# Kernel tuning notes

Hardware: AMD Instinct MI355X
Metric: run time of the kernel (lower is better)

Reference implementation:

```python
import jax, jax.numpy as jnp
import numpy as np

# dims: N batch, C in-channels, T frames, V joints, H heads, HD per-head dim, O out-channels
N, C, T, V = 32, 64, 256, 25
H, HD, O = 8, 8, 64  # HD = max(C//8, 8)
SCALE = HD ** -0.5
EPS = 1e-5


def setup_inputs() -> dict:
    key = jax.random.key(0)
    ks = jax.random.split(key, 10)
    return {
        "x": jax.random.normal(ks[0], (N, C, T, V), jnp.float32),
        "ln_gamma": jnp.ones((C,), jnp.float32),
        "ln_beta": jnp.zeros((C,), jnp.float32),
        "w_qk": jax.random.normal(ks[1], (C, 2 * H * HD), jnp.float32),  # to_qk init N(0,1)
        "b_qk": jax.random.normal(ks[2], (2 * H * HD,), jnp.float32) * 0.02,
        "shared_topology": jax.random.uniform(ks[3], (H, V, V), jnp.float32),
        "conv_w": jax.random.normal(ks[4], (H, O, C), jnp.float32) * np.sqrt(2.0 / (O * H)),
        "conv_b": jnp.zeros((H, O), jnp.float32),
        "bn_gamma": jnp.full((O,), 1e-6, jnp.float32),
        "bn_beta": jnp.zeros((O,), jnp.float32),
        "bn_mean": jnp.zeros((O,), jnp.float32),
        "bn_var": jnp.ones((O,), jnp.float32),
    }


def reference(x, ln_gamma, ln_beta, w_qk, b_qk, shared_topology,
              conv_w, conv_b, bn_gamma, bn_beta, bn_mean, bn_var):
    # ---- SelfAttention over joints ----
    y = jnp.transpose(x, (0, 2, 3, 1))                 # [N,T,V,C]
    mu = jnp.mean(y, axis=-1, keepdims=True)
    var = jnp.var(y, axis=-1, keepdims=True)
    yn = (y - mu) * jax.lax.rsqrt(var + EPS) * ln_gamma + ln_beta
    qk = yn @ w_qk + b_qk                              # [N,T,V,2*H*HD]
    B = N * T
    q, k = jnp.split(qk.reshape(B, V, 2 * H * HD), 2, axis=-1)
    q = q.reshape(B, V, H, HD).transpose(0, 2, 1, 3)   # [B,H,V,HD]
    k = k.reshape(B, V, H, HD).transpose(0, 2, 1, 3)
    dots = jnp.einsum("bhid,bhjd->bhij", q, k) * SCALE
    attn = jax.nn.softmax(dots, axis=-1).astype(jnp.float32)  # [B,H,V,V]

    # ---- attention-gated graph conv ----
    A = attn * shared_topology[None]                   # [B,H,V,V]
    feat = jnp.transpose(x, (0, 2, 3, 1)).reshape(B, V, C)  # [B,V,C]
    z = jnp.einsum("bhuv,bvc->bhuc", A, feat)          # per-head aggregate [B,H,V,C]
    # fused per-head 1x1 convs + sum over heads
    out = jnp.einsum("bhuc,hoc->buo", z, conv_w) + conv_b.sum(0)  # [B,V,O]
    out = out.reshape(N, T, V, O).transpose(0, 3, 1, 2)           # [N,O,T,V]

    # ---- BatchNorm (inference-mode) + residual + ReLU ----
    g = (bn_gamma * jax.lax.rsqrt(bn_var + EPS))[None, :, None, None]
    b = (bn_beta - bn_mean * bn_gamma * jax.lax.rsqrt(bn_var + EPS))[None, :, None, None]
    out = out * g + b
    out = jax.nn.relu(out + x)  # down is identity (in_c == out_c)
    return out
```

## Files before the change

kernel.cpp:

```cpp
#include <hip/hip_runtime.h>
#include <math.h>

#define SCALE 0.35355339059327373f
#define EPSV 1e-5f

typedef __attribute__((ext_vector_type(8))) short bf16x8;
typedef __attribute__((ext_vector_type(4))) float f32x4;
typedef __attribute__((ext_vector_type(16))) float f32x16;
typedef __attribute__((ext_vector_type(4))) int i32x4;
typedef __attribute__((ext_vector_type(2))) int i32x2;

static __device__ __forceinline__ unsigned short bfh(float f) {
    return (unsigned short)(__builtin_bit_cast(unsigned int, f) >> 16);
}
static __device__ __forceinline__ float bf2f(unsigned short s) {
    return __builtin_bit_cast(float, (unsigned int)s << 16);
}
static __device__ __forceinline__ int pack2(float lo, float hi) {
    return __builtin_amdgcn_perm(__builtin_bit_cast(unsigned int, hi),
                                 __builtin_bit_cast(unsigned int, lo), 0x07060302u);
}
#define LGKM0() __asm__ __volatile__("s_waitcnt lgkmcnt(0)" ::: "memory")

__global__ void prep_kernel(const float* __restrict__ w_qk,
                            const float* __restrict__ conv_w,
                            const float* __restrict__ conv_b,
                            const float* __restrict__ bn_g, const float* __restrict__ bn_b,
                            const float* __restrict__ bn_m, const float* __restrict__ bn_v,
                            unsigned short* __restrict__ ws) {
    int i = blockIdx.x * 256 + threadIdx.x;
    if (i < 8192) {
        int f = i >> 9, rem = i & 511, l = rem >> 3, j = rem & 7;
        int nt = f >> 1, ks = f & 1;
        int k = ks * 32 + (l >> 4) * 8 + j;
        int nn = nt * 16 + (l & 15);
        ws[i] = bfh(w_qk[k * 128 + nn]);
    } else if (i < 40960) {
        int i2 = i - 8192;
        int g = i2 >> 9, rem = i2 & 511, l = rem >> 3, j = rem & 7;
        int h = g >> 3, nt = (g >> 1) & 3, ks = g & 1;
        int c = ks * 32 + (l >> 4) * 8 + j;
        int o = nt * 16 + (l & 15);
        ws[i] = bfh(conv_w[h * 4096 + o * 64 + c]);
    } else if (i < 41024) {
        int o = i - 40960;
        float gv = bn_g[o] * rsqrtf(bn_v[o] + EPSV);
        float bb = bn_b[o] - bn_m[o] * gv;
        float cb = 0.f;
        for (int h = 0; h < 8; h++) cb += conv_b[h * 64 + o];
        float* wsf = (float*)(ws + 40960);
        wsf[o] = gv;
        wsf[64 + o] = bb + cb * gv;
    }
}

__global__ __launch_bounds__(256, 3)
void sagc_kernel(const float* __restrict__ x,
                 const float* __restrict__ ln_g, const float* __restrict__ ln_b,
                 const float* __restrict__ b_qk,
                 const float* __restrict__ topo,
                 const unsigned short* __restrict__ ws,
                 float* __restrict__ out)
{
    __shared__ __align__(16) unsigned char smem[53248];
    const int tid = threadIdx.x;
    const int lane = tid & 63, wv = tid >> 6;
    const int l15 = lane & 15, quad = lane >> 4;
    const int r32 = lane & 31, hi = lane >> 5;

    unsigned char* my = smem + wv * 13312;
    unsigned short* xb16 = (unsigned short*)my;
    unsigned short* FWT  = (unsigned short*)my;
    float*          mus  = (float*)(my + 5120);
    float*          rss  = mus + 32;
    unsigned short* qbuf = (unsigned short*)(my + 5120);
    unsigned short* kbuf = (unsigned short*)(my + 6656);
    unsigned short* Gh   = (unsigned short*)(my + 8192);

    const unsigned short* wqk = ws;
    const unsigned short* w2f = ws + 8192;
    const float* bnA = (const float*)(ws + 40960);
    const float* bnB = bnA + 64;

    const int tile = blockIdx.x * 4 + wv;
    const int n = tile >> 8, t = tile & 255;
    const float* xg = x + (size_t)n * 409600 + (size_t)t * 25;
    float* og = out + (size_t)n * 409600 + (size_t)t * 25;

    #pragma unroll
    for (int it = 0; it < 25; it++) {
        int i = it * 64 + lane;
        int c = i / 25, v = i - c * 25;
        xb16[v * 72 + c] = bfh(xg[c * 6400 + v]);
    }
    #pragma unroll
    for (int k = 0; k < 8; k++) {
        int idx = k * 64 + lane;
        if (idx < 504) {
            int rr = idx / 72, cc = idx - rr * 72;
            xb16[(25 + rr) * 72 + cc] = 0;
        }
    }
    LGKM0();

    bf16x8 xa[2][2];
    #pragma unroll
    for (int mt = 0; mt < 2; mt++)
        #pragma unroll
        for (int ks = 0; ks < 2; ks++)
            xa[mt][ks] = *(const bf16x8*)&xb16[(mt * 16 + l15) * 72 + ks * 32 + quad * 8];

    float xf[2][2][8];
    bf16x8 sqf[2][2];
    #pragma unroll
    for (int mt = 0; mt < 2; mt++)
        #pragma unroll
        for (int ks = 0; ks < 2; ks++) {
            float s[8];
            #pragma unroll
            for (int j = 0; j < 8; j++) {
                xf[mt][ks][j] = bf2f((unsigned short)xa[mt][ks][j]);
                s[j] = xf[mt][ks][j] * xf[mt][ks][j];
            }
            i32x4 p;
            #pragma unroll
            for (int q = 0; q < 4; q++) p[q] = pack2(s[2 * q], s[2 * q + 1]);
            sqf[mt][ks] = __builtin_bit_cast(bf16x8, p);
        }

    {
        i32x4 ones_i = {0x3C803C80, 0x3C803C80, 0x3C803C80, 0x3C803C80};
        bf16x8 onesf = __builtin_bit_cast(bf16x8, ones_i);
        f32x4 z4 = {0.f, 0.f, 0.f, 0.f};
        f32x4 dmu[2], ds2[2];
        #pragma unroll
        for (int mt = 0; mt < 2; mt++) {
            dmu[mt] = __builtin_amdgcn_mfma_f32_16x16x32_bf16(xa[mt][0], onesf, z4, 0, 0, 0);
            dmu[mt] = __builtin_amdgcn_mfma_f32_16x16x32_bf16(xa[mt][1], onesf, dmu[mt], 0, 0, 0);
            ds2[mt] = __builtin_amdgcn_mfma_f32_16x16x32_bf16(sqf[mt][0], onesf, z4, 0, 0, 0);
            ds2[mt] = __builtin_amdgcn_mfma_f32_16x16x32_bf16(sqf[mt][1], onesf, ds2[mt], 0, 0, 0);
        }
        if (l15 == 0) {
            #pragma unroll
            for (int mt = 0; mt < 2; mt++)
                #pragma unroll
                for (int r = 0; r < 4; r++) {
                    int v = mt * 16 + quad * 4 + r;
                    float mu = dmu[mt][r];
                    float var = ds2[mt][r] - mu * mu;
                    mus[v] = mu;
                    rss[v] = rsqrtf(var + EPSV);
                }
        }
    }
    LGKM0();

    bf16x8 yna[2][2];
    {
        float muv[2] = {mus[l15], mus[16 + l15]};
        float rsv[2] = {rss[l15], rss[16 + l15]};
        #pragma unroll
        for (int ks = 0; ks < 2; ks++) {
            f32x4 ga = *(const f32x4*)&ln_g[ks * 32 + quad * 8];
            f32x4 gb = *(const f32x4*)&ln_g[ks * 32 + quad * 8 + 4];
            f32x4 ba = *(const f32x4*)&ln_b[ks * 32 + quad * 8];
            f32x4 bb = *(const f32x4*)&ln_b[ks * 32 + quad * 8 + 4];
            #pragma unroll
            for (int mt = 0; mt < 2; mt++) {
                float yv[8];
                #pragma unroll
                for (int j = 0; j < 8; j++) {
                    float g = (j < 4) ? ga[j] : gb[j - 4];
                    float bt = (j < 4) ? ba[j] : bb[j - 4];
                    yv[j] = (xf[mt][ks][j] - muv[mt]) * rsv[mt] * g + bt;
                }
                i32x4 p;
                #pragma unroll
                for (int q = 0; q < 4; q++) p[q] = pack2(yv[2 * q], yv[2 * q + 1]);
                yna[mt][ks] = __builtin_bit_cast(bf16x8, p);
            }
        }
    }

    f32x4 acc[2][4];
    #pragma unroll
    for (int mt = 0; mt < 2; mt++)
        #pragma unroll
        for (int nt = 0; nt < 4; nt++)
            acc[mt][nt] = (f32x4){0.f, 0.f, 0.f, 0.f};

    const f32x4 z4 = {0.f, 0.f, 0.f, 0.f};
    const bf16x8 z8 = {0, 0, 0, 0, 0, 0, 0, 0};

    for (int hp = 0; hp < 4; hp++) {
        #pragma unroll
        for (int tsel = 0; tsel < 2; tsel++) {
            int nt = tsel ? (4 + hp) : hp;
            bf16x8 b0 = *(const bf16x8*)&wqk[(nt * 2 + 0) * 512 + lane * 8];
            bf16x8 b1 = *(const bf16x8*)&wqk[(nt * 2 + 1) * 512 + lane * 8];
            float bias = b_qk[(tsel ? 64 : 0) + hp * 16 + l15];
            unsigned short* buf = tsel ? kbuf : qbuf;
            #pragma unroll
            for (int mt = 0; mt < 2; mt++) {
                f32x4 d = __builtin_amdgcn_mfma_f32_16x16x32_bf16(yna[mt][0], b0, z4, 0, 0, 0);
                d = __builtin_amdgcn_mfma_f32_16x16x32_bf16(yna[mt][1], b1, d, 0, 0, 0);
                #pragma unroll
                for (int r = 0; r < 4; r++) {
                    int u = mt * 16 + quad * 4 + r;
                    if (u < 25) {
                        float val = d[r] + bias;
                        if (!tsel) val *= SCALE;
                        buf[u * 24 + l15] = bfh(val);
                    }
                }
            }
        }
        LGKM0();

        #pragma unroll
        for (int hh = 0; hh < 2; hh++) {
            bf16x8 aq = z8, bk = z8;
            if (hi == 0) {
                aq = *(const bf16x8*)&qbuf[r32 * 24 + hh * 8];
                bk = *(const bf16x8*)&kbuf[r32 * 24 + hh * 8];
            }
            f32x16 dd = {0.f,0.f,0.f,0.f,0.f,0.f,0.f,0.f,0.f,0.f,0.f,0.f,0.f,0.f,0.f,0.f};
            dd = __builtin_amdgcn_mfma_f32_32x32x16_bf16(aq, bk, dd, 0, 0, 0);
            #pragma unroll
            for (int r = 0; r < 16; r++) {
                int u = (r & 3) + 8 * (r >> 2) + 4 * hi;
                if (u < 25) Gh[hh * 1280 + u * 40 + r32] = bfh(dd[r]);
            }
        }
        LGKM0();

        {
            int smh = lane >> 5, su = lane & 31;
            if (su < 25) {
                unsigned short* rowp = Gh + smh * 1280 + su * 40;
                i32x4 ra = *(const i32x4*)rowp;
                i32x4 rb = *(const i32x4*)(rowp + 8);
                i32x4 rc = *(const i32x4*)(rowp + 16);
                float f[25];
                #pragma unroll
                for (int w = 0; w < 4; w++) {
                    f[2 * w]      = __builtin_bit_cast(float, (unsigned)ra[w] << 16);
                    f[2 * w + 1]  = __builtin_bit_cast(float, (unsigned)ra[w] & 0xFFFF0000u);
                    f[8 + 2 * w]  = __builtin_bit_cast(float, (unsigned)rb[w] << 16);
                    f[9 + 2 * w]  = __builtin_bit_cast(float, (unsigned)rb[w] & 0xFFFF0000u);
                    f[16 + 2 * w] = __builtin_bit_cast(float, (unsigned)rc[w] << 16);
                    f[17 + 2 * w] = __builtin_bit_cast(float, (unsigned)rc[w] & 0xFFFF0000u);
                }
                f[24] = bf2f(rowp[24]);
                float m = f[0];
                #pragma unroll
                for (int v = 1; v < 25; v++) m = fmaxf(m, f[v]);
                float s = 0.f;
                #pragma unroll
                for (int v = 0; v < 25; v++) { f[v] = __expf(f[v] - m); s += f[v]; }
                float inv = 1.0f / s;
                const float* tp = topo + (hp * 2 + smh) * 625 + su * 25;
                #pragma unroll
                for (int v = 0; v < 25; v++) f[v] = f[v] * inv * tp[v];
                int d[16];
                #pragma unroll
                for (int p = 0; p < 12; p++) d[p] = pack2(f[2 * p], f[2 * p + 1]);
                d[12] = pack2(f[24], 0.f);
                d[13] = 0; d[14] = 0; d[15] = 0;
                *(i32x4*)rowp        = (i32x4){d[0], d[1], d[2], d[3]};
                *(i32x4*)(rowp + 8)  = (i32x4){d[4], d[5], d[6], d[7]};
                *(i32x4*)(rowp + 16) = (i32x4){d[8], d[9], d[10], d[11]};
                *(i32x4*)(rowp + 24) = (i32x4){d[12], d[13], d[14], d[15]};
            }
        }
        LGKM0();

        #pragma unroll
        for (int hh = 0; hh < 2; hh++) {
            int h = hp * 2 + hh;
            #pragma unroll
            for (int nt = 0; nt < 4; nt++) {
                bf16x8 w0 = *(const bf16x8*)&w2f[((h * 4 + nt) * 2 + 0) * 512 + lane * 8];
                bf16x8 w1 = *(const bf16x8*)&w2f[((h * 4 + nt) * 2 + 1) * 512 + lane * 8];
                f32x4 dw0 = __builtin_amdgcn_mfma_f32_16x16x32_bf16(xa[0][0], w0, z4, 0, 0, 0);
                dw0 = __builtin_amdgcn_mfma_f32_16x16x32_bf16(xa[0][1], w1, dw0, 0, 0, 0);
                f32x4 dw1 = __builtin_amdgcn_mfma_f32_16x16x32_bf16(xa[1][0], w0, z4, 0, 0, 0);
                dw1 = __builtin_amdgcn_mfma_f32_16x16x32_bf16(xa[1][1], w1, dw1, 0, 0, 0);
                int o = nt * 16 + l15;
                i32x2 q0 = {pack2(dw0[0], dw0[1]), pack2(dw0[2], dw0[3])};
                i32x2 q1 = {pack2(dw1[0], dw1[1]), pack2(dw1[2], dw1[3])};
                *(i32x2*)&FWT[o * 40 + quad * 4] = q0;
                *(i32x2*)&FWT[o * 40 + 16 + quad * 4] = q1;
            }
            LGKM0();
            bf16x8 ag0 = *(const bf16x8*)&Gh[hh * 1280 + l15 * 40 + quad * 8];
            bf16x8 ag1 = *(const bf16x8*)&Gh[hh * 1280 + (16 + l15) * 40 + quad * 8];
            #pragma unroll
            for (int nt = 0; nt < 4; nt++) {
                bf16x8 br = *(const bf16x8*)&FWT[(nt * 16 + l15) * 40 + quad * 8];
                acc[0][nt] = __builtin_amdgcn_mfma_f32_16x16x32_bf16(ag0, br, acc[0][nt], 0, 0, 0);
                acc[1][nt] = __builtin_amdgcn_mfma_f32_16x16x32_bf16(ag1, br, acc[1][nt], 0, 0, 0);
            }
        }
    }

    #pragma unroll
    for (int nt = 0; nt < 4; nt++) {
        int o = nt * 16 + l15;
        float gA = bnA[o], gB = bnB[o];
        #pragma unroll
        for (int mt = 0; mt < 2; mt++) {
            int ub = mt * 16 + quad * 4;
            #pragma unroll
            for (int r = 0; r < 4; r++) {
                int u = ub + r;
                if (u < 25) {
                    float val = acc[mt][nt][r] * gA + gB + xg[o * 6400 + u];
                    og[o * 6400 + u] = fmaxf(val, 0.f);
                }
            }
        }
    }
}

extern "C" void kernel_launch(void* const* d_in, const int* in_sizes, int n_in,
                              void* d_out, int out_size, void* d_ws, size_t ws_size,
                              hipStream_t stream) {
    const float* x      = (const float*)d_in[0];
    const float* ln_g   = (const float*)d_in[1];
    const float* ln_b   = (const float*)d_in[2];
    const float* w_qk   = (const float*)d_in[3];
    const float* b_qk   = (const float*)d_in[4];
    const float* topo   = (const float*)d_in[5];
    const float* conv_w = (const float*)d_in[6];
    const float* conv_b = (const float*)d_in[7];
    const float* bn_g   = (const float*)d_in[8];
    const float* bn_b   = (const float*)d_in[9];
    const float* bn_m   = (const float*)d_in[10];
    const float* bn_v   = (const float*)d_in[11];
    float* outp = (float*)d_out;
    unsigned short* wsp = (unsigned short*)d_ws;

    hipLaunchKernelGGL(prep_kernel, dim3(161), dim3(256), 0, stream,
                       w_qk, conv_w, conv_b, bn_g, bn_b, bn_m, bn_v, wsp);
    hipLaunchKernelGGL(sagc_kernel, dim3(2048), dim3(256), 0, stream,
                       x, ln_g, ln_b, b_qk, topo, (const unsigned short*)wsp, outp);
}
```

Baseline: 189.1 us.

## Process one head per iteration to shrink LDS and raise occupancy

```diff
diff --git a/kernel.cpp b/kernel.cpp
--- a/kernel.cpp
+++ b/kernel.cpp
@@ -20,7 +20,6 @@
     return __builtin_amdgcn_perm(__builtin_bit_cast(unsigned int, hi),
                                  __builtin_bit_cast(unsigned int, lo), 0x07060302u);
 }
-#define LGKM0() __asm__ __volatile__("s_waitcnt lgkmcnt(0)" ::: "memory")
 
 __global__ void prep_kernel(const float* __restrict__ w_qk,
                             const float* __restrict__ conv_w,
@@ -34,7 +33,9 @@
         int nt = f >> 1, ks = f & 1;
         int k = ks * 32 + (l >> 4) * 8 + j;
         int nn = nt * 16 + (l & 15);
-        ws[i] = bfh(w_qk[k * 128 + nn]);
+        float w = w_qk[k * 128 + nn];
+        if (nt < 4) w *= SCALE;
+        ws[i] = bfh(w);
     } else if (i < 40960) {
         int i2 = i - 8192;
         int g = i2 >> 9, rem = i2 & 511, l = rem >> 3, j = rem & 7;
@@ -54,7 +55,7 @@
     }
 }
 
-__global__ __launch_bounds__(256, 3)
+__global__ __launch_bounds__(256, 4)
 void sagc_kernel(const float* __restrict__ x,
                  const float* __restrict__ ln_g, const float* __restrict__ ln_b,
                  const float* __restrict__ b_qk,
@@ -62,20 +63,20 @@
                  const unsigned short* __restrict__ ws,
                  float* __restrict__ out)
 {
-    __shared__ __align__(16) unsigned char smem[53248];
+    __shared__ __align__(16) unsigned char smem[38912];
     const int tid = threadIdx.x;
     const int lane = tid & 63, wv = tid >> 6;
     const int l15 = lane & 15, quad = lane >> 4;
     const int r32 = lane & 31, hi = lane >> 5;
 
-    unsigned char* my = smem + wv * 13312;
+    unsigned char* my = smem + wv * 9728;
     unsigned short* xb16 = (unsigned short*)my;
     unsigned short* FWT  = (unsigned short*)my;
     float*          mus  = (float*)(my + 5120);
     float*          rss  = mus + 32;
     unsigned short* qbuf = (unsigned short*)(my + 5120);
-    unsigned short* kbuf = (unsigned short*)(my + 6656);
-    unsigned short* Gh   = (unsigned short*)(my + 8192);
+    unsigned short* kbuf = (unsigned short*)(my + 6144);
+    unsigned short* Gh   = (unsigned short*)(my + 7168);
 
     const unsigned short* wqk = ws;
     const unsigned short* w2f = ws + 8192;
@@ -101,7 +102,6 @@
             xb16[(25 + rr) * 72 + cc] = 0;
         }
     }
-    LGKM0();
 
     bf16x8 xa[2][2];
     #pragma unroll
@@ -131,13 +131,13 @@
     {
         i32x4 ones_i = {0x3C803C80, 0x3C803C80, 0x3C803C80, 0x3C803C80};
         bf16x8 onesf = __builtin_bit_cast(bf16x8, ones_i);
-        f32x4 z4 = {0.f, 0.f, 0.f, 0.f};
+        f32x4 z4i = {0.f, 0.f, 0.f, 0.f};
         f32x4 dmu[2], ds2[2];
         #pragma unroll
         for (int mt = 0; mt < 2; mt++) {
-            dmu[mt] = __builtin_amdgcn_mfma_f32_16x16x32_bf16(xa[mt][0], onesf, z4, 0, 0, 0);
+            dmu[mt] = __builtin_amdgcn_mfma_f32_16x16x32_bf16(xa[mt][0], onesf, z4i, 0, 0, 0);
             dmu[mt] = __builtin_amdgcn_mfma_f32_16x16x32_bf16(xa[mt][1], onesf, dmu[mt], 0, 0, 0);
-            ds2[mt] = __builtin_amdgcn_mfma_f32_16x16x32_bf16(sqf[mt][0], onesf, z4, 0, 0, 0);
+            ds2[mt] = __builtin_amdgcn_mfma_f32_16x16x32_bf16(sqf[mt][0], onesf, z4i, 0, 0, 0);
             ds2[mt] = __builtin_amdgcn_mfma_f32_16x16x32_bf16(sqf[mt][1], onesf, ds2[mt], 0, 0, 0);
         }
         if (l15 == 0) {
@@ -153,7 +153,6 @@
                 }
         }
     }
-    LGKM0();
 
     bf16x8 yna[2][2];
     {
@@ -192,109 +191,100 @@
     const f32x4 z4 = {0.f, 0.f, 0.f, 0.f};
     const bf16x8 z8 = {0, 0, 0, 0, 0, 0, 0, 0};
 
-    for (int hp = 0; hp < 4; hp++) {
-        #pragma unroll
-        for (int tsel = 0; tsel < 2; tsel++) {
-            int nt = tsel ? (4 + hp) : hp;
-            bf16x8 b0 = *(const bf16x8*)&wqk[(nt * 2 + 0) * 512 + lane * 8];
-            bf16x8 b1 = *(const bf16x8*)&wqk[(nt * 2 + 1) * 512 + lane * 8];
-            float bias = b_qk[(tsel ? 64 : 0) + hp * 16 + l15];
-            unsigned short* buf = tsel ? kbuf : qbuf;
-            #pragma unroll
-            for (int mt = 0; mt < 2; mt++) {
-                f32x4 d = __builtin_amdgcn_mfma_f32_16x16x32_bf16(yna[mt][0], b0, z4, 0, 0, 0);
-                d = __builtin_amdgcn_mfma_f32_16x16x32_bf16(yna[mt][1], b1, d, 0, 0, 0);
+    for (int h = 0; h < 8; h++) {
+        const int hp = h >> 1, hl = h & 1;
+        if (hl == 0) {
+            #pragma unroll
+            for (int tsel = 0; tsel < 2; tsel++) {
+                int nt = tsel ? (4 + hp) : hp;
+                bf16x8 b0 = *(const bf16x8*)&wqk[(nt * 2 + 0) * 512 + lane * 8];
+                bf16x8 b1 = *(const bf16x8*)&wqk[(nt * 2 + 1) * 512 + lane * 8];
+                float bias = b_qk[(tsel ? 64 : 0) + hp * 16 + l15];
+                if (!tsel) bias *= SCALE;
+                unsigned short* buf = tsel ? kbuf : qbuf;
                 #pragma unroll
-                for (int r = 0; r < 4; r++) {
-                    int u = mt * 16 + quad * 4 + r;
-                    if (u < 25) {
-                        float val = d[r] + bias;
-                        if (!tsel) val *= SCALE;
-                        buf[u * 24 + l15] = bfh(val);
+                for (int mt = 0; mt < 2; mt++) {
+                    f32x4 d = __builtin_amdgcn_mfma_f32_16x16x32_bf16(yna[mt][0], b0, z4, 0, 0, 0);
+                    d = __builtin_amdgcn_mfma_f32_16x16x32_bf16(yna[mt][1], b1, d, 0, 0, 0);
+                    #pragma unroll
+                    for (int r = 0; r < 4; r++) {
+                        int u = mt * 16 + quad * 4 + r;
+                        if (u < 25) buf[u * 16 + l15] = bfh(d[r] + bias);
                     }
                 }
             }
         }
-        LGKM0();
-
-        #pragma unroll
-        for (int hh = 0; hh < 2; hh++) {
+
+        {
             bf16x8 aq = z8, bk = z8;
             if (hi == 0) {
-                aq = *(const bf16x8*)&qbuf[r32 * 24 + hh * 8];
-                bk = *(const bf16x8*)&kbuf[r32 * 24 + hh * 8];
+                aq = *(const bf16x8*)&qbuf[r32 * 16 + hl * 8];
+                bk = *(const bf16x8*)&kbuf[r32 * 16 + hl * 8];
             }
             f32x16 dd = {0.f,0.f,0.f,0.f,0.f,0.f,0.f,0.f,0.f,0.f,0.f,0.f,0.f,0.f,0.f,0.f};
             dd = __builtin_amdgcn_mfma_f32_32x32x16_bf16(aq, bk, dd, 0, 0, 0);
             #pragma unroll
             for (int r = 0; r < 16; r++) {
                 int u = (r & 3) + 8 * (r >> 2) + 4 * hi;
-                if (u < 25) Gh[hh * 1280 + u * 40 + r32] = bfh(dd[r]);
-            }
-        }
-        LGKM0();
+                if (u < 25) Gh[u * 40 + r32] = bfh(dd[r]);
+            }
+        }
+
+        #pragma unroll
+        for (int nt = 0; nt < 4; nt++) {
+            bf16x8 w0 = *(const bf16x8*)&w2f[((h * 4 + nt) * 2 + 0) * 512 + lane * 8];
+            bf16x8 w1 = *(const bf16x8*)&w2f[((h * 4 + nt) * 2 + 1) * 512 + lane * 8];
+            f32x4 dw0 = __builtin_amdgcn_mfma_f32_16x16x32_bf16(xa[0][0], w0, z4, 0, 0, 0);
+            dw0 = __builtin_amdgcn_mfma_f32_16x16x32_bf16(xa[0][1], w1, dw0, 0, 0, 0);
+            f32x4 dw1 = __builtin_amdgcn_mfma_f32_16x16x32_bf16(xa[1][0], w0, z4, 0, 0, 0);
+            dw1 = __builtin_amdgcn_mfma_f32_16x16x32_bf16(xa[1][1], w1, dw1, 0, 0, 0);
+            int o = nt * 16 + l15;
+            i32x2 q0 = {pack2(dw0[0], dw0[1]), pack2(dw0[2], dw0[3])};
+            i32x2 q1 = {pack2(dw1[0], dw1[1]), pack2(dw1[2], dw1[3])};
+            *(i32x2*)&FWT[o * 40 + quad * 4] = q0;
+            *(i32x2*)&FWT[o * 40 + 16 + quad * 4] = q1;
+        }
+
+        if (lane < 25) {
+            unsigned short* rowp = Gh + lane * 40;
+            i32x4 ra = *(const i32x4*)rowp;
+            i32x4 rb = *(const i32x4*)(rowp + 8);
+            i32x4 rc = *(const i32x4*)(rowp + 16);
+            float f[25];
+            #pragma unroll
+            for (int w = 0; w < 4; w++) {
+                f[2 * w]      = __builtin_bit_cast(float, (unsigned)ra[w] << 16);
+                f[2 * w + 1]  = __builtin_bit_cast(float, (unsigned)ra[w] & 0xFFFF0000u);
+                f[8 + 2 * w]  = __builtin_bit_cast(float, (unsigned)rb[w] << 16);
+                f[9 + 2 * w]  = __builtin_bit_cast(float, (unsigned)rb[w] & 0xFFFF0000u);
+                f[16 + 2 * w] = __builtin_bit_cast(float, (unsigned)rc[w] << 16);
+                f[17 + 2 * w] = __builtin_bit_cast(float, (unsigned)rc[w] & 0xFFFF0000u);
+            }
+            f[24] = bf2f(rowp[24]);
+            float m = f[0];
+            #pragma unroll
+            for (int v = 1; v < 25; v++) m = fmaxf(m, f[v]);
+            float s = 0.f;
+            #pragma unroll
+            for (int v = 0; v < 25; v++) { f[v] = __expf(f[v] - m); s += f[v]; }
+            float inv = 1.0f / s;
+            const float* tp = topo + h * 625 + lane * 25;
+            #pragma unroll
+            for (int v = 0; v < 25; v++) f[v] = f[v] * inv * tp[v];
+            int d[16];
+            #pragma unroll
+            for (int p = 0; p < 12; p++) d[p] = pack2(f[2 * p], f[2 * p + 1]);
+            d[12] = pack2(f[24], 0.f);
+            d[13] = 0; d[14] = 0; d[15] = 0;
+            *(i32x4*)rowp        = (i32x4){d[0], d[1], d[2], d[3]};
+            *(i32x4*)(rowp + 8)  = (i32x4){d[4], d[5], d[6], d[7]};
+            *(i32x4*)(rowp + 16) = (i32x4){d[8], d[9], d[10], d[11]};
+            *(i32x4*)(rowp + 24) = (i32x4){d[12], d[13], d[14], d[15]};
+        }
 
         {
-            int smh = lane >> 5, su = lane & 31;
-            if (su < 25) {
-                unsigned short* rowp = Gh + smh * 1280 + su * 40;
-                i32x4 ra = *(const i32x4*)rowp;
-                i32x4 rb = *(const i32x4*)(rowp + 8);
-                i32x4 rc = *(const i32x4*)(rowp + 16);
-                float f[25];
-                #pragma unroll
-                for (int w = 0; w < 4; w++) {
-                    f[2 * w]      = __builtin_bit_cast(float, (unsigned)ra[w] << 16);
-                    f[2 * w + 1]  = __builtin_bit_cast(float, (unsigned)ra[w] & 0xFFFF0000u);
-                    f[8 + 2 * w]  = __builtin_bit_cast(float, (unsigned)rb[w] << 16);
-                    f[9 + 2 * w]  = __builtin_bit_cast(float, (unsigned)rb[w] & 0xFFFF0000u);
-                    f[16 + 2 * w] = __builtin_bit_cast(float, (unsigned)rc[w] << 16);
-                    f[17 + 2 * w] = __builtin_bit_cast(float, (unsigned)rc[w] & 0xFFFF0000u);
-                }
-                f[24] = bf2f(rowp[24]);
-                float m = f[0];
-                #pragma unroll
-                for (int v = 1; v < 25; v++) m = fmaxf(m, f[v]);
-                float s = 0.f;
-                #pragma unroll
-                for (int v = 0; v < 25; v++) { f[v] = __expf(f[v] - m); s += f[v]; }
-                float inv = 1.0f / s;
-                const float* tp = topo + (hp * 2 + smh) * 625 + su * 25;
-                #pragma unroll
-                for (int v = 0; v < 25; v++) f[v] = f[v] * inv * tp[v];
-                int d[16];
-                #pragma unroll
-                for (int p = 0; p < 12; p++) d[p] = pack2(f[2 * p], f[2 * p + 1]);
-                d[12] = pack2(f[24], 0.f);
-                d[13] = 0; d[14] = 0; d[15] = 0;
-                *(i32x4*)rowp        = (i32x4){d[0], d[1], d[2], d[3]};
-                *(i32x4*)(rowp + 8)  = (i32x4){d[4], d[5], d[6], d[7]};
-                *(i32x4*)(rowp + 16) = (i32x4){d[8], d[9], d[10], d[11]};
-                *(i32x4*)(rowp + 24) = (i32x4){d[12], d[13], d[14], d[15]};
-            }
-        }
-        LGKM0();
-
-        #pragma unroll
-        for (int hh = 0; hh < 2; hh++) {
-            int h = hp * 2 + hh;
-            #pragma unroll
-            for (int nt = 0; nt < 4; nt++) {
-                bf16x8 w0 = *(const bf16x8*)&w2f[((h * 4 + nt) * 2 + 0) * 512 + lane * 8];
-                bf16x8 w1 = *(const bf16x8*)&w2f[((h * 4 + nt) * 2 + 1) * 512 + lane * 8];
-                f32x4 dw0 = __builtin_amdgcn_mfma_f32_16x16x32_bf16(xa[0][0], w0, z4, 0, 0, 0);
-                dw0 = __builtin_amdgcn_mfma_f32_16x16x32_bf16(xa[0][1], w1, dw0, 0, 0, 0);
-                f32x4 dw1 = __builtin_amdgcn_mfma_f32_16x16x32_bf16(xa[1][0], w0, z4, 0, 0, 0);
-                dw1 = __builtin_amdgcn_mfma_f32_16x16x32_bf16(xa[1][1], w1, dw1, 0, 0, 0);
-                int o = nt * 16 + l15;
-                i32x2 q0 = {pack2(dw0[0], dw0[1]), pack2(dw0[2], dw0[3])};
-                i32x2 q1 = {pack2(dw1[0], dw1[1]), pack2(dw1[2], dw1[3])};
-                *(i32x2*)&FWT[o * 40 + quad * 4] = q0;
-                *(i32x2*)&FWT[o * 40 + 16 + quad * 4] = q1;
-            }
-            LGKM0();
-            bf16x8 ag0 = *(const bf16x8*)&Gh[hh * 1280 + l15 * 40 + quad * 8];
-            bf16x8 ag1 = *(const bf16x8*)&Gh[hh * 1280 + (16 + l15) * 40 + quad * 8];
+            bf16x8 ag0 = *(const bf16x8*)&Gh[l15 * 40 + quad * 8];
+            bf16x8 ag1 = *(const bf16x8*)&Gh[(16 + l15) * 40 + quad * 8];
             #pragma unroll
             for (int nt = 0; nt < 4; nt++) {
                 bf16x8 br = *(const bf16x8*)&FWT[(nt * 16 + l15) * 40 + quad * 8];
```

Measured after the change: 234.0 us. +23.7%, slower.

## Fold weight preprocessing into main kernel and drop separate prep launch

Applied to the files above, without the earlier changes.

```diff
diff --git a/kernel.cpp b/kernel.cpp
--- a/kernel.cpp
+++ b/kernel.cpp
@@ -20,46 +20,22 @@
     return __builtin_amdgcn_perm(__builtin_bit_cast(unsigned int, hi),
                                  __builtin_bit_cast(unsigned int, lo), 0x07060302u);
 }
+static __device__ __forceinline__ bf16x8 pack8(const float* v) {
+    i32x4 p;
+    #pragma unroll
+    for (int q = 0; q < 4; q++) p[q] = pack2(v[2 * q], v[2 * q + 1]);
+    return __builtin_bit_cast(bf16x8, p);
+}
 #define LGKM0() __asm__ __volatile__("s_waitcnt lgkmcnt(0)" ::: "memory")
-
-__global__ void prep_kernel(const float* __restrict__ w_qk,
-                            const float* __restrict__ conv_w,
-                            const float* __restrict__ conv_b,
-                            const float* __restrict__ bn_g, const float* __restrict__ bn_b,
-                            const float* __restrict__ bn_m, const float* __restrict__ bn_v,
-                            unsigned short* __restrict__ ws) {
-    int i = blockIdx.x * 256 + threadIdx.x;
-    if (i < 8192) {
-        int f = i >> 9, rem = i & 511, l = rem >> 3, j = rem & 7;
-        int nt = f >> 1, ks = f & 1;
-        int k = ks * 32 + (l >> 4) * 8 + j;
-        int nn = nt * 16 + (l & 15);
-        ws[i] = bfh(w_qk[k * 128 + nn]);
-    } else if (i < 40960) {
-        int i2 = i - 8192;
-        int g = i2 >> 9, rem = i2 & 511, l = rem >> 3, j = rem & 7;
-        int h = g >> 3, nt = (g >> 1) & 3, ks = g & 1;
-        int c = ks * 32 + (l >> 4) * 8 + j;
-        int o = nt * 16 + (l & 15);
-        ws[i] = bfh(conv_w[h * 4096 + o * 64 + c]);
-    } else if (i < 41024) {
-        int o = i - 40960;
-        float gv = bn_g[o] * rsqrtf(bn_v[o] + EPSV);
-        float bb = bn_b[o] - bn_m[o] * gv;
-        float cb = 0.f;
-        for (int h = 0; h < 8; h++) cb += conv_b[h * 64 + o];
-        float* wsf = (float*)(ws + 40960);
-        wsf[o] = gv;
-        wsf[64 + o] = bb + cb * gv;
-    }
-}
 
 __global__ __launch_bounds__(256, 3)
 void sagc_kernel(const float* __restrict__ x,
                  const float* __restrict__ ln_g, const float* __restrict__ ln_b,
-                 const float* __restrict__ b_qk,
+                 const float* __restrict__ w_qk, const float* __restrict__ b_qk,
                  const float* __restrict__ topo,
-                 const unsigned short* __restrict__ ws,
+                 const float* __restrict__ conv_w, const float* __restrict__ conv_b,
+                 const float* __restrict__ bn_g, const float* __restrict__ bn_b,
+                 const float* __restrict__ bn_m, const float* __restrict__ bn_v,
                  float* __restrict__ out)
 {
     __shared__ __align__(16) unsigned char smem[53248];
@@ -77,11 +53,6 @@
     unsigned short* kbuf = (unsigned short*)(my + 6656);
     unsigned short* Gh   = (unsigned short*)(my + 8192);
 
-    const unsigned short* wqk = ws;
-    const unsigned short* w2f = ws + 8192;
-    const float* bnA = (const float*)(ws + 40960);
-    const float* bnB = bnA + 64;
-
     const int tile = blockIdx.x * 4 + wv;
     const int n = tile >> 8, t = tile & 255;
     const float* xg = x + (size_t)n * 409600 + (size_t)t * 25;
@@ -122,22 +93,19 @@
                 xf[mt][ks][j] = bf2f((unsigned short)xa[mt][ks][j]);
                 s[j] = xf[mt][ks][j] * xf[mt][ks][j];
             }
-            i32x4 p;
-            #pragma unroll
-            for (int q = 0; q < 4; q++) p[q] = pack2(s[2 * q], s[2 * q + 1]);
-            sqf[mt][ks] = __builtin_bit_cast(bf16x8, p);
+            sqf[mt][ks] = pack8(s);
         }
 
     {
         i32x4 ones_i = {0x3C803C80, 0x3C803C80, 0x3C803C80, 0x3C803C80};
         bf16x8 onesf = __builtin_bit_cast(bf16x8, ones_i);
-        f32x4 z4 = {0.f, 0.f, 0.f, 0.f};
+        f32x4 z4i = {0.f, 0.f, 0.f, 0.f};
         f32x4 dmu[2], ds2[2];
         #pragma unroll
         for (int mt = 0; mt < 2; mt++) {
-            dmu[mt] = __builtin_amdgcn_mfma_f32_16x16x32_bf16(xa[mt][0], onesf, z4, 0, 0, 0);
+            dmu[mt] = __builtin_amdgcn_mfma_f32_16x16x32_bf16(xa[mt][0], onesf, z4i, 0, 0, 0);
             dmu[mt] = __builtin_amdgcn_mfma_f32_16x16x32_bf16(xa[mt][1], onesf, dmu[mt], 0, 0, 0);
-            ds2[mt] = __builtin_amdgcn_mfma_f32_16x16x32_bf16(sqf[mt][0], onesf, z4, 0, 0, 0);
+            ds2[mt] = __builtin_amdgcn_mfma_f32_16x16x32_bf16(sqf[mt][0], onesf, z4i, 0, 0, 0);
             ds2[mt] = __builtin_amdgcn_mfma_f32_16x16x32_bf16(sqf[mt][1], onesf, ds2[mt], 0, 0, 0);
         }
         if (l15 == 0) {
@@ -174,10 +142,7 @@
                     float bt = (j < 4) ? ba[j] : bb[j - 4];
                     yv[j] = (xf[mt][ks][j] - muv[mt]) * rsv[mt] * g + bt;
                 }
-                i32x4 p;
-                #pragma unroll
-                for (int q = 0; q < 4; q++) p[q] = pack2(yv[2 * q], yv[2 * q + 1]);
-                yna[mt][ks] = __builtin_bit_cast(bf16x8, p);
+                yna[mt][ks] = pack8(yv);
             }
         }
     }
@@ -196,9 +161,21 @@
         #pragma unroll
         for (int tsel = 0; tsel < 2; tsel++) {
             int nt = tsel ? (4 + hp) : hp;
-            bf16x8 b0 = *(const bf16x8*)&wqk[(nt * 2 + 0) * 512 + lane * 8];
-            bf16x8 b1 = *(const bf16x8*)&wqk[(nt * 2 + 1) * 512 + lane * 8];
+            const float* wp = w_qk + quad * 8 * 128 + nt * 16 + l15;
+            float w0v[8], w1v[8];
+            #pragma unroll
+            for (int j = 0; j < 8; j++) {
+                w0v[j] = wp[j * 128];
+                w1v[j] = wp[(32 + j) * 128];
+            }
+            if (!tsel) {
+                #pragma unroll
+                for (int j = 0; j < 8; j++) { w0v[j] *= SCALE; w1v[j] *= SCALE; }
+            }
+            bf16x8 b0 = pack8(w0v);
+            bf16x8 b1 = pack8(w1v);
             float bias = b_qk[(tsel ? 64 : 0) + hp * 16 + l15];
+            if (!tsel) bias *= SCALE;
             unsigned short* buf = tsel ? kbuf : qbuf;
             #pragma unroll
             for (int mt = 0; mt < 2; mt++) {
@@ -207,11 +184,7 @@
                 #pragma unroll
                 for (int r = 0; r < 4; r++) {
                     int u = mt * 16 + quad * 4 + r;
-                    if (u < 25) {
-                        float val = d[r] + bias;
-                        if (!tsel) val *= SCALE;
-                        buf[u * 24 + l15] = bfh(val);
-                    }
+                    if (u < 25) buf[u * 24 + l15] = bfh(d[r] + bias);
                 }
             }
         }
@@ -280,8 +253,15 @@
             int h = hp * 2 + hh;
             #pragma unroll
             for (int nt = 0; nt < 4; nt++) {
-                bf16x8 w0 = *(const bf16x8*)&w2f[((h * 4 + nt) * 2 + 0) * 512 + lane * 8];
-                bf16x8 w1 = *(const bf16x8*)&w2f[((h * 4 + nt) * 2 + 1) * 512 + lane * 8];
+                const float* cp = conv_w + h * 4096 + (nt * 16 + l15) * 64 + quad * 8;
+                f32x4 c0 = *(const f32x4*)cp;
+                f32x4 c1 = *(const f32x4*)(cp + 4);
+                f32x4 c2 = *(const f32x4*)(cp + 32);
+                f32x4 c3 = *(const f32x4*)(cp + 36);
+                float wv0[8] = {c0[0], c0[1], c0[2], c0[3], c1[0], c1[1], c1[2], c1[3]};
+                float wv1[8] = {c2[0], c2[1], c2[2], c2[3], c3[0], c3[1], c3[2], c3[3]};
+                bf16x8 w0 = pack8(wv0);
+                bf16x8 w1 = pack8(wv1);
                 f32x4 dw0 = __builtin_amdgcn_mfma_f32_16x16x32_bf16(xa[0][0], w0, z4, 0, 0, 0);
                 dw0 = __builtin_amdgcn_mfma_f32_16x16x32_bf16(xa[0][1], w1, dw0, 0, 0, 0);
                 f32x4 dw1 = __builtin_amdgcn_mfma_f32_16x16x32_bf16(xa[1][0], w0, z4, 0, 0, 0);
@@ -307,7 +287,11 @@
     #pragma unroll
     for (int nt = 0; nt < 4; nt++) {
         int o = nt * 16 + l15;
-        float gA = bnA[o], gB = bnB[o];
+        float gA = bn_g[o] * rsqrtf(bn_v[o] + EPSV);
+        float cb = 0.f;
+        #pragma unroll
+        for (int h = 0; h < 8; h++) cb += conv_b[h * 64 + o];
+        float gB = bn_b[o] - bn_m[o] * gA + cb * gA;
         #pragma unroll
         for (int mt = 0; mt < 2; mt++) {
             int ub = mt * 16 + quad * 4;
@@ -339,10 +323,8 @@
     const float* bn_m   = (const float*)d_in[10];
     const float* bn_v   = (const float*)d_in[11];
     float* outp = (float*)d_out;
-    unsigned short* wsp = (unsigned short*)d_ws;
-
-    hipLaunchKernelGGL(prep_kernel, dim3(161), dim3(256), 0, stream,
-                       w_qk, conv_w, conv_b, bn_g, bn_b, bn_m, bn_v, wsp);
+
     hipLaunchKernelGGL(sagc_kernel, dim3(2048), dim3(256), 0, stream,
-                       x, ln_g, ln_b, b_qk, topo, (const unsigned short*)wsp, outp);
-}
+                       x, ln_g, ln_b, w_qk, b_qk, topo, conv_w, conv_b,
+                       bn_g, bn_b, bn_m, bn_v, outp);
+}
```

Result: slower. 290.2 us (+53.5%).
